# Performance work log

Measured on AMD Instinct MI355X. Metric: run time of the kernel, lower is better.

The kernel has to match this reference:

```python
import jax, jax.numpy as jnp
import numpy as np

BS, S, H, T = 16, 256, 1024, 32  # batch, num entities, hidden, num relation tags
N_TAGS = 7


def setup_inputs() -> dict:
    key = jax.random.key(0)
    k0, k1, k2, k3 = jax.random.split(key, 4)
    seq_embedding = jax.random.normal(k0, (BS, H), dtype=jnp.float32)
    entities_embeddings = jax.random.normal(k1, (BS, S, H), dtype=jnp.float32)
    entities_tags = jax.random.randint(k2, (BS, S), 0, N_TAGS)
    # relation_classifier: Linear(3*H -> T)
    W = jax.random.normal(k3, (T, 3 * H), dtype=jnp.float32) * 0.02
    b = jnp.zeros((T,), dtype=jnp.float32)
    return {
        "seq_embedding": seq_embedding,
        "entities_embeddings": entities_embeddings,
        "W": W,
        "b": b,
        "entities_tags": entities_tags,
    }


def reference(seq_embedding, entities_embeddings, W, b, entities_tags):
    # Original (eval mode, dropout=identity):
    #   pred[b,i,j] = W @ concat(E[b,i], E[b,j], S[b]) + bias
    # (arg1/arg2/all_seq linears and tag embeddings are dead code in the
    #  original forward: their outputs are never used.)
    # Decompose W = [W1 | W2 | W3] along the feature axis; mathematically
    # identical to materializing the (bs,S,S,3H) concat tensor.
    h = entities_embeddings.shape[-1]
    W1, W2, W3 = W[:, :h], W[:, h:2 * h], W[:, 2 * h:]
    p1 = jnp.einsum('bih,th->bit', entities_embeddings, W1)  # arg1 contribution
    p2 = jnp.einsum('bjh,th->bjt', entities_embeddings, W2)  # arg2 contribution
    ps = seq_embedding @ W3.T + b                             # seq + bias
    # (bs, S, S, T)
    return p1[:, :, None, :] + p2[:, None, :, :] + ps[:, None, None, :]
```

## Files before the change

kernel.cpp:

```cpp
#include <hip/hip_runtime.h>

#define BS 16
#define S  256
#define H  1024
#define T  32

#define PS_OFF 0
#define P1_OFF 512
#define P2_OFF (P1_OFF + BS * S * T)

typedef __bf16 bf16x8 __attribute__((ext_vector_type(8)));
typedef float  f32x4  __attribute__((ext_vector_type(4)));

__device__ inline bf16x8 to_bf8(float4 lo, float4 hi) {
    bf16x8 r;
    r[0] = (__bf16)lo.x; r[1] = (__bf16)lo.y; r[2] = (__bf16)lo.z; r[3] = (__bf16)lo.w;
    r[4] = (__bf16)hi.x; r[5] = (__bf16)hi.y; r[6] = (__bf16)hi.z; r[7] = (__bf16)hi.w;
    return r;
}

__global__ __launch_bounds__(512) void gemm_ps(
    const float* __restrict__ seq, const float* __restrict__ E,
    const float* __restrict__ W, const float* __restrict__ bias,
    float* __restrict__ ws)
{
    const int tid = threadIdx.x;
    const int lane = tid & 63, wv = tid >> 6;

    if (blockIdx.x < 64) {
        float* ps = ws + PS_OFF;
        const int o = blockIdx.x * 8 + wv;
        const int bb = o >> 5, t = o & 31;
        const float4* sp = (const float4*)(seq + (size_t)bb * H) + lane * 4;
        const float4* wp = (const float4*)(W + (size_t)t * (3 * H) + 2 * H) + lane * 4;
        float acc = 0.f;
        #pragma unroll
        for (int k = 0; k < 4; ++k) {
            float4 a = sp[k], w = wp[k];
            acc += a.x * w.x + a.y * w.y + a.z * w.z + a.w * w.w;
        }
        #pragma unroll
        for (int m = 32; m >= 1; m >>= 1) acc += __shfl_xor(acc, m);
        if (lane == 0) ps[o] = acc + bias[t];
        return;
    }

    __shared__ __align__(16) __bf16 Ebf[16][1032];
    __shared__ __align__(16) float  pacc[2][16][64];

    const int m0 = (blockIdx.x - 64) * 16;
    const int kc = wv >> 2;
    const int cg = wv & 3;
    const int kbeg = kc * 512;

    float4 tmpa[4], tmpb[4];
    #pragma unroll
    for (int i = 0; i < 4; ++i) {
        int c = tid + i * 512;
        int row = c >> 7, c8 = c & 127;
        const float4* src = (const float4*)(E + (size_t)(m0 + row) * H + c8 * 8);
        tmpa[i] = src[0]; tmpb[i] = src[1];
    }

    const int col = cg * 16 + (lane & 15);
    const int ksub = (lane >> 4) * 8;
    const float* wbase = W + (size_t)(col & 31) * (3 * H)
                           + ((col >= 32) ? H : 0) + kbeg + ksub;
    bf16x8 bfrag[16];
    #pragma unroll
    for (int s = 0; s < 16; ++s)
        bfrag[s] = to_bf8(*(const float4*)(wbase + s * 32),
                          *(const float4*)(wbase + s * 32 + 4));

    #pragma unroll
    for (int i = 0; i < 4; ++i) {
        int c = tid + i * 512;
        int row = c >> 7, c8 = c & 127;
        *(bf16x8*)&Ebf[row][c8 * 8] = to_bf8(tmpa[i], tmpb[i]);
    }
    __syncthreads();

    f32x4 acc = {0.f, 0.f, 0.f, 0.f};
    const int erow = lane & 15;
    #pragma unroll
    for (int s = 0; s < 16; ++s) {
        bf16x8 a = *(const bf16x8*)&Ebf[erow][kbeg + s * 32 + ksub];
        acc = __builtin_amdgcn_mfma_f32_16x16x32_bf16(a, bfrag[s], acc, 0, 0, 0);
    }

    const int orow = (lane >> 4) * 4;
    #pragma unroll
    for (int r = 0; r < 4; ++r)
        pacc[kc][orow + r][col] = acc[r];
    __syncthreads();

    #pragma unroll
    for (int e = tid; e < 1024; e += 512) {
        const int row = e >> 6, c = e & 63;
        float v = pacc[0][row][c] + pacc[1][row][c];
        if (c < 32) (ws + P1_OFF)[(size_t)(m0 + row) * T + c] = v;
        else        (ws + P2_OFF)[(size_t)(m0 + row) * T + (c - 32)] = v;
    }
}

__global__ __launch_bounds__(256) void bcast_add(
    const float* __restrict__ ws, float* __restrict__ out)
{
    const int blk = blockIdx.x;
    const int b = blk >> 8, i = blk & 255;
    const int tid = threadIdx.x;

    const float4 s1v = *(const float4*)((ws + P1_OFF)
                       + (size_t)(b * S + i) * T + (tid & 7) * 4);
    const float4 psv = *(const float4*)((ws + PS_OFF) + b * T + (tid & 7) * 4);
    float4 s;
    s.x = s1v.x + psv.x; s.y = s1v.y + psv.y;
    s.z = s1v.z + psv.z; s.w = s1v.w + psv.w;

    const float4* p2v = (const float4*)(ws + P2_OFF) + (size_t)b * (S * T / 4);
    float4* ov = (float4*)out + (size_t)(b * S + i) * (S * T / 4);

    #pragma unroll
    for (int k = tid; k < S * T / 4; k += 256) {
        float4 v = p2v[k];
        float4 r;
        r.x = v.x + s.x; r.y = v.y + s.y; r.z = v.z + s.z; r.w = v.w + s.w;
        ov[k] = r;
    }
}

extern "C" void kernel_launch(void* const* d_in, const int* in_sizes, int n_in,
                              void* d_out, int out_size, void* d_ws, size_t ws_size,
                              hipStream_t stream)
{
    const float* seq  = (const float*)d_in[0];
    const float* E    = (const float*)d_in[1];
    const float* W    = (const float*)d_in[2];
    const float* bias = (const float*)d_in[3];
    float* out = (float*)d_out;
    float* ws  = (float*)d_ws;

    gemm_ps<<<320, 512, 0, stream>>>(seq, E, W, bias, ws);
    bcast_add<<<BS * S, 256, 0, stream>>>(ws, out);
}
```

Measured before the change: 37.93 us.

## Fuse projection GEMM and broadcast-add into one kernel with per-batch atomic flags

Merges the GEMM/ps kernel and the broadcast-add kernel into a single 1024-block launch. Blocks signal completion per batch through release atomics, and each block spin-waits until its batch's 24 producers are done before writing its 4 output rows. The GEMM is restructured so one 256-thread block covers the full K per 16 rows, with no cross-wave reduction. This removes a kernel launch boundary but adds a memset launch and relies on the producer blocks being scheduled ahead of waiting consumers, which risks deadlock if they are not.

```diff
diff --git a/kernel.cpp b/kernel.cpp
--- a/kernel.cpp
+++ b/kernel.cpp
@@ -5,9 +5,11 @@
 #define H  1024
 #define T  32
 
-#define PS_OFF 0
-#define P1_OFF 512
-#define P2_OFF (P1_OFF + BS * S * T)
+#define PS_OFF  0
+#define P1_OFF  512
+#define P2_OFF  (P1_OFF + BS * S * T)
+#define CNT_OFF (P2_OFF + BS * S * T)
+#define TARGET  24u
 
 typedef __bf16 bf16x8 __attribute__((ext_vector_type(8)));
 typedef float  f32x4  __attribute__((ext_vector_type(4)));
@@ -19,17 +21,79 @@
     return r;
 }
 
-__global__ __launch_bounds__(512) void gemm_ps(
+__global__ __launch_bounds__(256, 4) void fused(
     const float* __restrict__ seq, const float* __restrict__ E,
     const float* __restrict__ W, const float* __restrict__ bias,
-    float* __restrict__ ws)
+    float* __restrict__ ws, float* __restrict__ out)
 {
     const int tid = threadIdx.x;
     const int lane = tid & 63, wv = tid >> 6;
+    const int blk = blockIdx.x;
+    unsigned* cnt = (unsigned*)(ws + CNT_OFF);
 
-    if (blockIdx.x < 64) {
+    __shared__ __align__(16) __bf16 Ebf[16][1032];
+
+    if (blk < 256) {
+        const int m0 = blk * 16;
+        #pragma unroll
+        for (int h = 0; h < 2; ++h) {
+            float4 ta[4], tb[4];
+            #pragma unroll
+            for (int i = 0; i < 4; ++i) {
+                int c = tid + i * 256;
+                int row = c >> 6, c8 = c & 63;
+                const float4* src = (const float4*)(E + (size_t)(m0 + row) * H
+                                                    + h * 512 + c8 * 8);
+                ta[i] = src[0]; tb[i] = src[1];
+            }
+            #pragma unroll
+            for (int i = 0; i < 4; ++i) {
+                int c = tid + i * 256;
+                int row = c >> 6, c8 = c & 63;
+                *(bf16x8*)&Ebf[row][h * 512 + c8 * 8] = to_bf8(ta[i], tb[i]);
+            }
+        }
+        __syncthreads();
+
+        const int col = wv * 16 + (lane & 15);
+        const int ksub = (lane >> 4) * 8;
+        const float* wbase = W + (size_t)(col & 31) * (3 * H)
+                               + ((col >= 32) ? H : 0) + ksub;
+        const int erow = lane & 15;
+        f32x4 accA = {0.f,0.f,0.f,0.f}, accB = {0.f,0.f,0.f,0.f};
+        #pragma unroll
+        for (int ch = 0; ch < 4; ++ch) {
+            bf16x8 bf[8];
+            #pragma unroll
+            for (int s = 0; s < 8; ++s)
+                bf[s] = to_bf8(*(const float4*)(wbase + ch * 256 + s * 32),
+                               *(const float4*)(wbase + ch * 256 + s * 32 + 4));
+            #pragma unroll
+            for (int s = 0; s < 8; s += 2) {
+                bf16x8 a0 = *(const bf16x8*)&Ebf[erow][ch * 256 + s * 32 + ksub];
+                bf16x8 a1 = *(const bf16x8*)&Ebf[erow][ch * 256 + (s+1) * 32 + ksub];
+                accA = __builtin_amdgcn_mfma_f32_16x16x32_bf16(a0, bf[s],   accA, 0, 0, 0);
+                accB = __builtin_amdgcn_mfma_f32_16x16x32_bf16(a1, bf[s+1], accB, 0, 0, 0);
+            }
+        }
+        f32x4 acc = accA + accB;
+
+        const int orow = (lane >> 4) * 4;
+        float* dst = (wv < 2) ? (ws + P1_OFF) : (ws + P2_OFF);
+        const int c = col & 31;
+        #pragma unroll
+        for (int r = 0; r < 4; ++r)
+            dst[(size_t)(m0 + orow + r) * T + c] = acc[r];
+
+        __syncthreads();
+        if (tid == 0) {
+            __threadfence();
+            __hip_atomic_fetch_add(&cnt[blk >> 4], 1u,
+                                   __ATOMIC_RELEASE, __HIP_MEMORY_SCOPE_AGENT);
+        }
+    } else if (blk < 384) {
         float* ps = ws + PS_OFF;
-        const int o = blockIdx.x * 8 + wv;
+        const int o = (blk - 256) * 4 + wv;
         const int bb = o >> 5, t = o & 31;
         const float4* sp = (const float4*)(seq + (size_t)bb * H) + lane * 4;
         const float4* wp = (const float4*)(W + (size_t)t * (3 * H) + 2 * H) + lane * 4;
@@ -42,90 +106,41 @@
         #pragma unroll
         for (int m = 32; m >= 1; m >>= 1) acc += __shfl_xor(acc, m);
         if (lane == 0) ps[o] = acc + bias[t];
-        return;
+        __syncthreads();
+        if (tid == 0) {
+            __threadfence();
+            __hip_atomic_fetch_add(&cnt[(blk - 256) >> 3], 1u,
+                                   __ATOMIC_RELEASE, __HIP_MEMORY_SCOPE_AGENT);
+        }
     }
 
-    __shared__ __align__(16) __bf16 Ebf[16][1032];
-    __shared__ __align__(16) float  pacc[2][16][64];
+    const int r0 = blk * 4;
+    const int b = blk >> 6;
 
-    const int m0 = (blockIdx.x - 64) * 16;
-    const int kc = wv >> 2;
-    const int cg = wv & 3;
-    const int kbeg = kc * 512;
-
-    float4 tmpa[4], tmpb[4];
-    #pragma unroll
-    for (int i = 0; i < 4; ++i) {
-        int c = tid + i * 512;
-        int row = c >> 7, c8 = c & 127;
-        const float4* src = (const float4*)(E + (size_t)(m0 + row) * H + c8 * 8);
-        tmpa[i] = src[0]; tmpb[i] = src[1];
-    }
-
-    const int col = cg * 16 + (lane & 15);
-    const int ksub = (lane >> 4) * 8;
-    const float* wbase = W + (size_t)(col & 31) * (3 * H)
-                           + ((col >= 32) ? H : 0) + kbeg + ksub;
-    bf16x8 bfrag[16];
-    #pragma unroll
-    for (int s = 0; s < 16; ++s)
-        bfrag[s] = to_bf8(*(const float4*)(wbase + s * 32),
-                          *(const float4*)(wbase + s * 32 + 4));
-
-    #pragma unroll
-    for (int i = 0; i < 4; ++i) {
-        int c = tid + i * 512;
-        int row = c >> 7, c8 = c & 127;
-        *(bf16x8*)&Ebf[row][c8 * 8] = to_bf8(tmpa[i], tmpb[i]);
+    if (tid == 0) {
+        while (__hip_atomic_load(&cnt[b], __ATOMIC_ACQUIRE,
+                                 __HIP_MEMORY_SCOPE_AGENT) < TARGET)
+            __builtin_amdgcn_s_sleep(8);
     }
     __syncthreads();
 
-    f32x4 acc = {0.f, 0.f, 0.f, 0.f};
-    const int erow = lane & 15;
+    const float4* p2v = (const float4*)(ws + P2_OFF) + (size_t)b * (S * T / 4);
+    const float4 psv = *(const float4*)((ws + PS_OFF) + b * T + (tid & 7) * 4);
     #pragma unroll
-    for (int s = 0; s < 16; ++s) {
-        bf16x8 a = *(const bf16x8*)&Ebf[erow][kbeg + s * 32 + ksub];
-        acc = __builtin_amdgcn_mfma_f32_16x16x32_bf16(a, bfrag[s], acc, 0, 0, 0);
-    }
-
-    const int orow = (lane >> 4) * 4;
-    #pragma unroll
-    for (int r = 0; r < 4; ++r)
-        pacc[kc][orow + r][col] = acc[r];
-    __syncthreads();
-
-    #pragma unroll
-    for (int e = tid; e < 1024; e += 512) {
-        const int row = e >> 6, c = e & 63;
-        float v = pacc[0][row][c] + pacc[1][row][c];
-        if (c < 32) (ws + P1_OFF)[(size_t)(m0 + row) * T + c] = v;
-        else        (ws + P2_OFF)[(size_t)(m0 + row) * T + (c - 32)] = v;
-    }
-}
-
-__global__ __launch_bounds__(256) void bcast_add(
-    const float* __restrict__ ws, float* __restrict__ out)
-{
-    const int blk = blockIdx.x;
-    const int b = blk >> 8, i = blk & 255;
-    const int tid = threadIdx.x;
-
-    const float4 s1v = *(const float4*)((ws + P1_OFF)
-                       + (size_t)(b * S + i) * T + (tid & 7) * 4);
-    const float4 psv = *(const float4*)((ws + PS_OFF) + b * T + (tid & 7) * 4);
-    float4 s;
-    s.x = s1v.x + psv.x; s.y = s1v.y + psv.y;
-    s.z = s1v.z + psv.z; s.w = s1v.w + psv.w;
-
-    const float4* p2v = (const float4*)(ws + P2_OFF) + (size_t)b * (S * T / 4);
-    float4* ov = (float4*)out + (size_t)(b * S + i) * (S * T / 4);
-
-    #pragma unroll
-    for (int k = tid; k < S * T / 4; k += 256) {
-        float4 v = p2v[k];
-        float4 r;
-        r.x = v.x + s.x; r.y = v.y + s.y; r.z = v.z + s.z; r.w = v.w + s.w;
-        ov[k] = r;
+    for (int rr = 0; rr < 4; ++rr) {
+        const size_t row = r0 + rr;
+        float4 s1v = *(const float4*)((ws + P1_OFF) + row * T + (tid & 7) * 4);
+        float4 s;
+        s.x = s1v.x + psv.x; s.y = s1v.y + psv.y;
+        s.z = s1v.z + psv.z; s.w = s1v.w + psv.w;
+        float4* ov = (float4*)out + row * (S * T / 4);
+        #pragma unroll
+        for (int k = tid; k < S * T / 4; k += 256) {
+            float4 v = p2v[k];
+            float4 r;
+            r.x = v.x + s.x; r.y = v.y + s.y; r.z = v.z + s.z; r.w = v.w + s.w;
+            ov[k] = r;
+        }
     }
 }
 
@@ -140,6 +155,7 @@
     float* out = (float*)d_out;
     float* ws  = (float*)d_ws;
 
-    gemm_ps<<<320, 512, 0, stream>>>(seq, E, W, bias, ws);
-    bcast_add<<<BS * S, 256, 0, stream>>>(ws, out);
+    hipMemsetAsync((void*)((char*)d_ws + (size_t)CNT_OFF * sizeof(float)), 0,
+                   16 * sizeof(unsigned), stream);
+    fused<<<1024, 256, 0, stream>>>(seq, E, W, bias, ws, out);
 }
```

New measurement: 125.0 us. 230% more time.
